# Kernel tuning notes

Hardware: AMD Instinct MI355X
Metric: run time of the kernel (lower is better)

The kernel has to match this reference:

```python
import jax, jax.numpy as jnp
import numpy as np


def setup_inputs() -> dict:
    key = jax.random.key(0)
    ks = jax.random.split(key, 5)
    B, Cin, Ch, H, W, K = 8, 64, 64, 128, 128, 3
    fan_in = (Cin + Ch) * K * K
    return {
        "x": jax.random.normal(ks[0], (B, Cin, H, W), jnp.float32),
        "prev_h": jax.random.normal(ks[1], (B, Ch, H, W), jnp.float32),
        "prev_c": jax.random.normal(ks[2], (B, Ch, H, W), jnp.float32),
        "W_gates": jax.random.normal(ks[3], (4 * Ch, Cin + Ch, K, K), jnp.float32) / np.sqrt(fan_in),
        "b_gates": jax.random.normal(ks[4], (4 * Ch,), jnp.float32) * 0.01,
    }


def reference(x, prev_h, prev_c, W_gates, b_gates):
    # ConvLSTM cell: conv over concat(input, prev_h) -> 4 gates -> gating.
    pad = W_gates.shape[-1] // 2
    stacked = jnp.concatenate([x, prev_h], axis=1)  # [B, Cin+Ch, H, W]
    gates = jax.lax.conv_general_dilated(
        stacked, W_gates,
        window_strides=(1, 1),
        padding=[(pad, pad), (pad, pad)],
        dimension_numbers=("NCHW", "OIHW", "NCHW"),
    ) + b_gates[None, :, None, None]  # [B, 4*Ch, H, W]
    in_gate, remember_gate, out_gate, cell_gate = jnp.split(gates, 4, axis=1)
    in_gate = jax.nn.sigmoid(in_gate)
    remember_gate = jax.nn.sigmoid(remember_gate)
    out_gate = jax.nn.sigmoid(out_gate)
    cell_gate = jnp.tanh(cell_gate)
    cell = in_gate * cell_gate + remember_gate * prev_c
    hidden = out_gate * jnp.tanh(cell)
    return (hidden, cell)
```

## Files before the change

### kernel.cpp

```cpp
#include <hip/hip_runtime.h>

typedef __attribute__((ext_vector_type(8))) short short8;
typedef __attribute__((ext_vector_type(4))) short short4v;
typedef __attribute__((ext_vector_type(4))) float float4v;

#define NPIX_HID 8388608
#define PST 132

__device__ __forceinline__ short f2bf(float f) {
    union { float f; unsigned u; } v; v.f = f;
    unsigned r = (v.u + 0x7FFFu + ((v.u >> 16) & 1u)) >> 16;
    return (short)r;
}

__device__ __forceinline__ float sigmoidf_(float v) { return 1.f / (1.f + __expf(-v)); }
__device__ __forceinline__ float tanhf_(float v)    { return 2.f / (1.f + __expf(-2.f * v)) - 1.f; }

__global__ void wprep(const float* __restrict__ W, short* __restrict__ A) {
    int tid = blockIdx.x * 256 + threadIdx.x;
    if (tid >= 9 * 16 * 256 * 8) return;
    int j   = tid & 7;
    int co  = (tid >> 3) & 255;
    int cig = (tid >> 11) & 15;
    int kk  = tid >> 15;
    int ci  = cig * 8 + j;
    A[tid] = f2bf(W[co * 1152 + ci * 9 + kk]);
}

#define ST_LOAD(P, II)                                                        \
  {                                                                           \
    const int i_ = (II);                                                      \
    P##_act = (i_ < 4224);                                                    \
    const int px_ = i_ % 66;                                                  \
    const int ro_ = i_ / 66;                                                  \
    P##_oct = ro_ & 15;                                                       \
    P##_row = ro_ >> 4;                                                       \
    const int ys_ = y0 + P##_row - 1;                                         \
    const int xs_ = x0 + px_ - 1;                                             \
    P##_px = px_;                                                             \
    P##_ok = P##_act & ((unsigned)ys_ < 128u) & ((unsigned)xs_ < 128u);       \
    const float* src_ = (P##_oct < 8) ? x : ph;                               \
    const float* sp_ = src_ + (P##_ok ?                                       \
        (((b * 64 + (P##_oct & 7) * 8) * 128 + ys_) * 128 + xs_) : 0);        \
    P##_v[0] = sp_[0];        P##_v[1] = sp_[16384];                          \
    P##_v[2] = sp_[2 * 16384]; P##_v[3] = sp_[3 * 16384];                     \
    P##_v[4] = sp_[4 * 16384]; P##_v[5] = sp_[5 * 16384];                     \
    P##_v[6] = sp_[6 * 16384]; P##_v[7] = sp_[7 * 16384];                     \
  }

#define ST_PROC(P)                                                            \
  if (P##_act) {                                                              \
    short4v lo_ = {0,0,0,0}, hi_ = {0,0,0,0};                                 \
    if (P##_ok) {                                                             \
      lo_[0] = f2bf(P##_v[0]); lo_[1] = f2bf(P##_v[1]);                       \
      lo_[2] = f2bf(P##_v[2]); lo_[3] = f2bf(P##_v[3]);                       \
      hi_[0] = f2bf(P##_v[4]); hi_[1] = f2bf(P##_v[5]);                       \
      hi_[2] = f2bf(P##_v[6]); hi_[3] = f2bf(P##_v[7]);                       \
    }                                                                         \
    short* dst_ = &Bs[(P##_row * 66 + P##_px) * PST + P##_oct * 8];           \
    *(short4v*)dst_       = lo_;                                              \
    *(short4v*)(dst_ + 4) = hi_;                                              \
  }

__global__ __launch_bounds__(256, 2) void convlstm_main(
    const float* __restrict__ x, const float* __restrict__ ph,
    const float* __restrict__ pc, const short* __restrict__ aprep,
    const float* __restrict__ bg, float* __restrict__ out)
{
    __shared__ short Bs[4 * 66 * PST];

    const int tid  = threadIdx.x;
    const int lane = tid & 63;
    const int wave = tid >> 6;
    const int l15  = lane & 15;
    const int quad = lane >> 4;

    const int t  = blockIdx.x;
    const int x0 = (t & 1) * 64;
    const int y0 = ((t >> 1) & 63) * 2;
    const int b  = t >> 7;

    {
        float stA_v[8]; int stA_px, stA_row, stA_oct; bool stA_ok, stA_act;
        float stB_v[8]; int stB_px, stB_row, stB_oct; bool stB_ok, stB_act;
        int ib = tid;
        ST_LOAD(stA, ib);
#pragma unroll 1
        for (int it = 0; it < 16; it += 2) {
            ST_LOAD(stB, ib + 256);
            ST_PROC(stA);
            ST_LOAD(stA, ib + 512);
            ST_PROC(stB);
            ib += 512;
        }
        ST_PROC(stA);
    }
    __syncthreads();

    float4v acc[4][8];
#pragma unroll
    for (int mt = 0; mt < 4; ++mt)
#pragma unroll
        for (int nt = 0; nt < 8; ++nt)
            acc[mt][nt] = (float4v){0.f, 0.f, 0.f, 0.f};

    const short* ap = aprep + quad * 2048 + (wave * 16 + l15) * 8;
    short8 abuf[2][4];
#pragma unroll
    for (int mt = 0; mt < 4; ++mt) abuf[0][mt] = *(const short8*)(ap + mt * 512);

    const short* bb = &Bs[l15 * PST + quad * 8];
    short8 bfr[2][8];
#pragma unroll
    for (int nt = 0; nt < 8; ++nt) {
        const short* bp = bb + (nt >> 2) * (66 * PST) + (nt & 3) * (16 * PST);
        short4v lo = *(const short4v*)bp;
        short4v hi = *(const short4v*)(bp + 4);
        bfr[0][nt] = __builtin_shufflevector(lo, hi, 0, 1, 2, 3, 4, 5, 6, 7);
    }

#pragma unroll 1
    for (int ky = 0; ky < 3; ++ky) {
#pragma unroll 1
        for (int kx = 0; kx < 3; ++kx) {
            const bool lastkx = (ky == 2) & (kx == 2);
            const short* bbn = bb + ((kx == 2) ? 64 * PST : PST);
#pragma unroll
            for (int kc = 0; kc < 4; ++kc) {
                const int cur = kc & 1, nxt = cur ^ 1;
                const bool last = lastkx & (kc == 3);

                const short* apn = last ? ap : (ap + 8192);
#pragma unroll
                for (int mt = 0; mt < 4; ++mt)
                    abuf[nxt][mt] = *(const short8*)(apn + mt * 512);
                ap = apn;

                const short* bq = (kc == 3) ? (lastkx ? bb : bbn) : bb;
                const int kcn = (kc + 1) & 3;
#pragma unroll
                for (int nt = 0; nt < 8; ++nt) {
                    const short* bp = bq + (nt >> 2) * (66 * PST) + (nt & 3) * (16 * PST) + kcn * 32;
                    short4v lo = *(const short4v*)bp;
                    short4v hi = *(const short4v*)(bp + 4);
                    bfr[nxt][nt] = __builtin_shufflevector(lo, hi, 0, 1, 2, 3, 4, 5, 6, 7);
                }

                __builtin_amdgcn_s_setprio(1);
#pragma unroll
                for (int mt = 0; mt < 4; ++mt)
#pragma unroll
                    for (int nt = 0; nt < 8; ++nt)
                        acc[mt][nt] = __builtin_amdgcn_mfma_f32_16x16x32_bf16(
                            abuf[cur][mt], bfr[cur][nt], acc[mt][nt], 0, 0, 0);
                __builtin_amdgcn_s_setprio(0);
            }
            bb = bbn;
        }
    }

    float pcv[8][4];
#pragma unroll
    for (int nt = 0; nt < 8; ++nt) {
        const int y  = y0 + (nt >> 2);
        const int px = x0 + ((nt & 3) << 4) + l15;
#pragma unroll
        for (int r = 0; r < 4; ++r) {
            const int c = wave * 16 + quad * 4 + r;
            pcv[nt][r] = pc[((b * 64 + c) * 128 + y) * 128 + px];
        }
    }
#pragma unroll
    for (int nt = 0; nt < 8; ++nt) {
        const int y  = y0 + (nt >> 2);
        const int px = x0 + ((nt & 3) << 4) + l15;
#pragma unroll
        for (int r = 0; r < 4; ++r) {
            const int c = wave * 16 + quad * 4 + r;
            const float gi = acc[0][nt][r] + bg[c];
            const float gf = acc[1][nt][r] + bg[64 + c];
            const float go = acc[2][nt][r] + bg[128 + c];
            const float gc = acc[3][nt][r] + bg[192 + c];
            const float ig = sigmoidf_(gi);
            const float fg = sigmoidf_(gf);
            const float og = sigmoidf_(go);
            const float cg = tanhf_(gc);
            const int idx = ((b * 64 + c) * 128 + y) * 128 + px;
            const float cell = ig * cg + fg * pcv[nt][r];
            const float hid  = og * tanhf_(cell);
            out[idx] = hid;
            out[NPIX_HID + idx] = cell;
        }
    }
}

extern "C" void kernel_launch(void* const* d_in, const int* in_sizes, int n_in,
                              void* d_out, int out_size, void* d_ws, size_t ws_size,
                              hipStream_t stream) {
    const float* x  = (const float*)d_in[0];
    const float* ph = (const float*)d_in[1];
    const float* pc = (const float*)d_in[2];
    const float* W  = (const float*)d_in[3];
    const float* bg = (const float*)d_in[4];
    float* out = (float*)d_out;
    short* aprep = (short*)d_ws;

    wprep<<<1152, 256, 0, stream>>>(W, aprep);
    convlstm_main<<<1024, 256, 0, stream>>>(x, ph, pc, aprep, bg, out);
}
```

Baseline: 209.3 us.

## Process four output rows per block with a rolling LDS row buffer

Each block now computes four output rows using a 4-slot circular shared-memory buffer of input rows. The next halo row is prefetched into registers during the current row's MFMA loop and written afterwards. This cuts redundant halo loads and fp32-to-bf16 conversion, and hoists the bias loads. In exchange the grid is halved, a barrier is added per row, and the per-wave N tile shrinks from 8 to 4, which lowers reuse of each A fragment.

```diff
diff --git a/kernel.cpp b/kernel.cpp
--- a/kernel.cpp
+++ b/kernel.cpp
@@ -6,6 +6,7 @@
 
 #define NPIX_HID 8388608
 #define PST 132
+#define ROWPITCH (66 * PST)
 
 __device__ __forceinline__ short f2bf(float f) {
     union { float f; unsigned u; } v; v.f = f;
@@ -27,10 +28,10 @@
     A[tid] = f2bf(W[co * 1152 + ci * 9 + kk]);
 }
 
-#define ST_LOAD(P, II)                                                        \
+#define PRO_LOAD(P, II)                                                       \
   {                                                                           \
     const int i_ = (II);                                                      \
-    P##_act = (i_ < 4224);                                                    \
+    P##_act = (i_ < 3168);                                                    \
     const int px_ = i_ % 66;                                                  \
     const int ro_ = i_ / 66;                                                  \
     P##_oct = ro_ & 15;                                                       \
@@ -42,24 +43,58 @@
     const float* src_ = (P##_oct < 8) ? x : ph;                               \
     const float* sp_ = src_ + (P##_ok ?                                       \
         (((b * 64 + (P##_oct & 7) * 8) * 128 + ys_) * 128 + xs_) : 0);        \
-    P##_v[0] = sp_[0];        P##_v[1] = sp_[16384];                          \
-    P##_v[2] = sp_[2 * 16384]; P##_v[3] = sp_[3 * 16384];                     \
-    P##_v[4] = sp_[4 * 16384]; P##_v[5] = sp_[5 * 16384];                     \
-    P##_v[6] = sp_[6 * 16384]; P##_v[7] = sp_[7 * 16384];                     \
-  }
-
-#define ST_PROC(P)                                                            \
+    P##_v[0]=sp_[0]; P##_v[1]=sp_[16384]; P##_v[2]=sp_[2*16384];              \
+    P##_v[3]=sp_[3*16384]; P##_v[4]=sp_[4*16384]; P##_v[5]=sp_[5*16384];      \
+    P##_v[6]=sp_[6*16384]; P##_v[7]=sp_[7*16384];                             \
+  }
+
+#define PRO_PROC(P)                                                           \
   if (P##_act) {                                                              \
-    short4v lo_ = {0,0,0,0}, hi_ = {0,0,0,0};                                 \
+    short4v lo_={0,0,0,0}, hi_={0,0,0,0};                                     \
     if (P##_ok) {                                                             \
-      lo_[0] = f2bf(P##_v[0]); lo_[1] = f2bf(P##_v[1]);                       \
-      lo_[2] = f2bf(P##_v[2]); lo_[3] = f2bf(P##_v[3]);                       \
-      hi_[0] = f2bf(P##_v[4]); hi_[1] = f2bf(P##_v[5]);                       \
-      hi_[2] = f2bf(P##_v[6]); hi_[3] = f2bf(P##_v[7]);                       \
+      lo_[0]=f2bf(P##_v[0]); lo_[1]=f2bf(P##_v[1]);                           \
+      lo_[2]=f2bf(P##_v[2]); lo_[3]=f2bf(P##_v[3]);                           \
+      hi_[0]=f2bf(P##_v[4]); hi_[1]=f2bf(P##_v[5]);                           \
+      hi_[2]=f2bf(P##_v[6]); hi_[3]=f2bf(P##_v[7]);                           \
     }                                                                         \
-    short* dst_ = &Bs[(P##_row * 66 + P##_px) * PST + P##_oct * 8];           \
-    *(short4v*)dst_       = lo_;                                              \
-    *(short4v*)(dst_ + 4) = hi_;                                              \
+    short* dst_ = &Bs[(((P##_row + 3) & 3) * 66 + P##_px) * PST + P##_oct * 8]; \
+    *(short4v*)dst_ = lo_; *(short4v*)(dst_+4) = hi_;                         \
+  }
+
+#define IST_LOAD(P, K)                                                        \
+  {                                                                           \
+    const int i_ = tid + (K) * 256;                                           \
+    const int px_ = i_ % 66;                                                  \
+    const int oct_ = (i_ / 66) & 15;                                          \
+    const int xs_ = x0 + px_ - 1;                                             \
+    const bool ok_ = (i_ < 1056) & ((unsigned)ysrc < 128u)                    \
+                     & ((unsigned)xs_ < 128u);                                \
+    const float* src_ = (oct_ < 8) ? x : ph;                                  \
+    const float* sp_ = src_ + (ok_ ?                                          \
+        (((b * 64 + (oct_ & 7) * 8) * 128 + ysrc) * 128 + xs_) : 0);          \
+    P##_v[0]=sp_[0]; P##_v[1]=sp_[16384]; P##_v[2]=sp_[2*16384];              \
+    P##_v[3]=sp_[3*16384]; P##_v[4]=sp_[4*16384]; P##_v[5]=sp_[5*16384];      \
+    P##_v[6]=sp_[6*16384]; P##_v[7]=sp_[7*16384];                             \
+  }
+
+#define IST_WRITE(P, K)                                                       \
+  {                                                                           \
+    const int i_ = tid + (K) * 256;                                           \
+    if (i_ < 1056) {                                                          \
+      const int px_ = i_ % 66;                                                \
+      const int oct_ = i_ / 66;                                               \
+      const int xs_ = x0 + px_ - 1;                                           \
+      const bool ok_ = ((unsigned)ysrc < 128u) & ((unsigned)xs_ < 128u);      \
+      short4v lo_={0,0,0,0}, hi_={0,0,0,0};                                   \
+      if (ok_) {                                                              \
+        lo_[0]=f2bf(P##_v[0]); lo_[1]=f2bf(P##_v[1]);                         \
+        lo_[2]=f2bf(P##_v[2]); lo_[3]=f2bf(P##_v[3]);                         \
+        hi_[0]=f2bf(P##_v[4]); hi_[1]=f2bf(P##_v[5]);                         \
+        hi_[2]=f2bf(P##_v[6]); hi_[3]=f2bf(P##_v[7]);                         \
+      }                                                                       \
+      short* dst_ = &Bs[(wslot * 66 + px_) * PST + oct_ * 8];                 \
+      *(short4v*)dst_ = lo_; *(short4v*)(dst_+4) = hi_;                       \
+    }                                                                         \
   }
 
 __global__ __launch_bounds__(256, 2) void convlstm_main(
@@ -67,7 +102,7 @@
     const float* __restrict__ pc, const short* __restrict__ aprep,
     const float* __restrict__ bg, float* __restrict__ out)
 {
-    __shared__ short Bs[4 * 66 * PST];
+    __shared__ short Bs[4 * ROWPITCH];
 
     const int tid  = threadIdx.x;
     const int lane = tid & 63;
@@ -77,119 +112,150 @@
 
     const int t  = blockIdx.x;
     const int x0 = (t & 1) * 64;
-    const int y0 = ((t >> 1) & 63) * 2;
-    const int b  = t >> 7;
+    const int y0 = ((t >> 1) & 31) * 4;
+    const int b  = t >> 6;
 
     {
-        float stA_v[8]; int stA_px, stA_row, stA_oct; bool stA_ok, stA_act;
-        float stB_v[8]; int stB_px, stB_row, stB_oct; bool stB_ok, stB_act;
+        float pA_v[8]; int pA_px, pA_row, pA_oct; bool pA_ok, pA_act;
+        float pB_v[8]; int pB_px, pB_row, pB_oct; bool pB_ok, pB_act;
         int ib = tid;
-        ST_LOAD(stA, ib);
-#pragma unroll 1
-        for (int it = 0; it < 16; it += 2) {
-            ST_LOAD(stB, ib + 256);
-            ST_PROC(stA);
-            ST_LOAD(stA, ib + 512);
-            ST_PROC(stB);
+        PRO_LOAD(pA, ib);
+#pragma unroll 1
+        for (int it = 0; it < 12; it += 2) {
+            PRO_LOAD(pB, ib + 256);
+            PRO_PROC(pA);
+            PRO_LOAD(pA, ib + 512);
+            PRO_PROC(pB);
             ib += 512;
         }
-        ST_PROC(stA);
+        PRO_PROC(pA);
     }
     __syncthreads();
 
-    float4v acc[4][8];
-#pragma unroll
-    for (int mt = 0; mt < 4; ++mt)
-#pragma unroll
-        for (int nt = 0; nt < 8; ++nt)
-            acc[mt][nt] = (float4v){0.f, 0.f, 0.f, 0.f};
-
-    const short* ap = aprep + quad * 2048 + (wave * 16 + l15) * 8;
+    const short* ap_base = aprep + quad * 2048 + (wave * 16 + l15) * 8;
+    const short* ap = ap_base;
     short8 abuf[2][4];
 #pragma unroll
-    for (int mt = 0; mt < 4; ++mt) abuf[0][mt] = *(const short8*)(ap + mt * 512);
-
-    const short* bb = &Bs[l15 * PST + quad * 8];
-    short8 bfr[2][8];
-#pragma unroll
-    for (int nt = 0; nt < 8; ++nt) {
-        const short* bp = bb + (nt >> 2) * (66 * PST) + (nt & 3) * (16 * PST);
+    for (int mt = 0; mt < 4; ++mt) abuf[0][mt] = *(const short8*)(ap_base + mt * 512);
+
+    const int lqoff = l15 * PST + quad * 8;
+    const short* bb = &Bs[3 * ROWPITCH + lqoff];
+    short8 bfr[2][4];
+#pragma unroll
+    for (int nt = 0; nt < 4; ++nt) {
+        const short* bp = bb + nt * (16 * PST);
         short4v lo = *(const short4v*)bp;
         short4v hi = *(const short4v*)(bp + 4);
         bfr[0][nt] = __builtin_shufflevector(lo, hi, 0, 1, 2, 3, 4, 5, 6, 7);
     }
 
-#pragma unroll 1
-    for (int ky = 0; ky < 3; ++ky) {
-#pragma unroll 1
-        for (int kx = 0; kx < 3; ++kx) {
-            const bool lastkx = (ky == 2) & (kx == 2);
-            const short* bbn = bb + ((kx == 2) ? 64 * PST : PST);
-#pragma unroll
-            for (int kc = 0; kc < 4; ++kc) {
-                const int cur = kc & 1, nxt = cur ^ 1;
-                const bool last = lastkx & (kc == 3);
-
-                const short* apn = last ? ap : (ap + 8192);
-#pragma unroll
-                for (int mt = 0; mt < 4; ++mt)
-                    abuf[nxt][mt] = *(const short8*)(apn + mt * 512);
-                ap = apn;
-
-                const short* bq = (kc == 3) ? (lastkx ? bb : bbn) : bb;
-                const int kcn = (kc + 1) & 3;
-#pragma unroll
-                for (int nt = 0; nt < 8; ++nt) {
-                    const short* bp = bq + (nt >> 2) * (66 * PST) + (nt & 3) * (16 * PST) + kcn * 32;
-                    short4v lo = *(const short4v*)bp;
-                    short4v hi = *(const short4v*)(bp + 4);
-                    bfr[nxt][nt] = __builtin_shufflevector(lo, hi, 0, 1, 2, 3, 4, 5, 6, 7);
+    float bgv[4][4];
+#pragma unroll
+    for (int g = 0; g < 4; ++g)
+#pragma unroll
+        for (int r = 0; r < 4; ++r)
+            bgv[g][r] = bg[g * 64 + wave * 16 + quad * 4 + r];
+
+#pragma unroll 1
+    for (int yy = 0; yy < 4; ++yy) {
+        const int ysrc  = y0 + yy + 2;
+        const int wslot = (yy + 2) & 3;
+        const short* bbnext = &Bs[(yy & 3) * ROWPITCH + lqoff];
+
+        float st0_v[8], st1_v[8], st2_v[8], st3_v[8], st4_v[8];
+        if (yy < 3) {
+            IST_LOAD(st0, 0) IST_LOAD(st1, 1) IST_LOAD(st2, 2)
+            IST_LOAD(st3, 3) IST_LOAD(st4, 4)
+        }
+        const int y = y0 + yy;
+        float pcv[4][4];
+#pragma unroll
+        for (int nt = 0; nt < 4; ++nt) {
+            const int px = x0 + (nt << 4) + l15;
+#pragma unroll
+            for (int r = 0; r < 4; ++r) {
+                const int c = wave * 16 + quad * 4 + r;
+                pcv[nt][r] = pc[((b * 64 + c) * 128 + y) * 128 + px];
+            }
+        }
+
+        float4v acc[4][4];
+#pragma unroll
+        for (int mt = 0; mt < 4; ++mt)
+#pragma unroll
+            for (int nt = 0; nt < 4; ++nt)
+                acc[mt][nt] = (float4v){0.f, 0.f, 0.f, 0.f};
+
+#pragma unroll 1
+        for (int ky = 0; ky < 3; ++ky) {
+            const int scur = (yy + ky + 3) & 3;
+            const int snxt = (yy + ky) & 3;
+            const int dj = (snxt - scur) * 66 - 2;
+#pragma unroll 1
+            for (int kx = 0; kx < 3; ++kx) {
+                const bool lastkx = (ky == 2) & (kx == 2);
+                const short* bbn = bb + ((kx == 2) ? dj * PST : PST);
+#pragma unroll
+                for (int kc = 0; kc < 4; ++kc) {
+                    const int cur = kc & 1, nxt = cur ^ 1;
+                    const bool last = lastkx & (kc == 3);
+
+                    const short* apn = last ? ap_base : (ap + 8192);
+#pragma unroll
+                    for (int mt = 0; mt < 4; ++mt)
+                        abuf[nxt][mt] = *(const short8*)(apn + mt * 512);
+                    ap = apn;
+
+                    const short* bq = (kc == 3) ? (lastkx ? bbnext : bbn) : bb;
+                    const int kcn = (kc + 1) & 3;
+#pragma unroll
+                    for (int nt = 0; nt < 4; ++nt) {
+                        const short* bp = bq + nt * (16 * PST) + kcn * 32;
+                        short4v lo = *(const short4v*)bp;
+                        short4v hi = *(const short4v*)(bp + 4);
+                        bfr[nxt][nt] = __builtin_shufflevector(lo, hi, 0, 1, 2, 3, 4, 5, 6, 7);
+                    }
+
+                    __builtin_amdgcn_s_setprio(1);
+#pragma unroll
+                    for (int mt = 0; mt < 4; ++mt)
+#pragma unroll
+                        for (int nt = 0; nt < 4; ++nt)
+                            acc[mt][nt] = __builtin_amdgcn_mfma_f32_16x16x32_bf16(
+                                abuf[cur][mt], bfr[cur][nt], acc[mt][nt], 0, 0, 0);
+                    __builtin_amdgcn_s_setprio(0);
                 }
-
-                __builtin_amdgcn_s_setprio(1);
-#pragma unroll
-                for (int mt = 0; mt < 4; ++mt)
-#pragma unroll
-                    for (int nt = 0; nt < 8; ++nt)
-                        acc[mt][nt] = __builtin_amdgcn_mfma_f32_16x16x32_bf16(
-                            abuf[cur][mt], bfr[cur][nt], acc[mt][nt], 0, 0, 0);
-                __builtin_amdgcn_s_setprio(0);
+                bb = bbn;
             }
-            bb = bbn;
-        }
-    }
-
-    float pcv[8][4];
-#pragma unroll
-    for (int nt = 0; nt < 8; ++nt) {
-        const int y  = y0 + (nt >> 2);
-        const int px = x0 + ((nt & 3) << 4) + l15;
-#pragma unroll
-        for (int r = 0; r < 4; ++r) {
-            const int c = wave * 16 + quad * 4 + r;
-            pcv[nt][r] = pc[((b * 64 + c) * 128 + y) * 128 + px];
-        }
-    }
-#pragma unroll
-    for (int nt = 0; nt < 8; ++nt) {
-        const int y  = y0 + (nt >> 2);
-        const int px = x0 + ((nt & 3) << 4) + l15;
-#pragma unroll
-        for (int r = 0; r < 4; ++r) {
-            const int c = wave * 16 + quad * 4 + r;
-            const float gi = acc[0][nt][r] + bg[c];
-            const float gf = acc[1][nt][r] + bg[64 + c];
-            const float go = acc[2][nt][r] + bg[128 + c];
-            const float gc = acc[3][nt][r] + bg[192 + c];
-            const float ig = sigmoidf_(gi);
-            const float fg = sigmoidf_(gf);
-            const float og = sigmoidf_(go);
-            const float cg = tanhf_(gc);
-            const int idx = ((b * 64 + c) * 128 + y) * 128 + px;
-            const float cell = ig * cg + fg * pcv[nt][r];
-            const float hid  = og * tanhf_(cell);
-            out[idx] = hid;
-            out[NPIX_HID + idx] = cell;
+        }
+        bb = bbnext;
+
+        if (yy < 3) {
+            IST_WRITE(st0, 0) IST_WRITE(st1, 1) IST_WRITE(st2, 2)
+            IST_WRITE(st3, 3) IST_WRITE(st4, 4)
+        }
+        __syncthreads();
+
+#pragma unroll
+        for (int nt = 0; nt < 4; ++nt) {
+            const int px = x0 + (nt << 4) + l15;
+#pragma unroll
+            for (int r = 0; r < 4; ++r) {
+                const int c = wave * 16 + quad * 4 + r;
+                const float gi = acc[0][nt][r] + bgv[0][r];
+                const float gf = acc[1][nt][r] + bgv[1][r];
+                const float go = acc[2][nt][r] + bgv[2][r];
+                const float gc = acc[3][nt][r] + bgv[3][r];
+                const float ig = sigmoidf_(gi);
+                const float fg = sigmoidf_(gf);
+                const float og = sigmoidf_(go);
+                const float cg = tanhf_(gc);
+                const int idx = ((b * 64 + c) * 128 + y) * 128 + px;
+                const float cell = ig * cg + fg * pcv[nt][r];
+                const float hid  = og * tanhf_(cell);
+                out[idx] = hid;
+                out[NPIX_HID + idx] = cell;
+            }
         }
     }
 }
@@ -206,5 +272,5 @@
     short* aprep = (short*)d_ws;
 
     wprep<<<1152, 256, 0, stream>>>(W, aprep);
-    convlstm_main<<<1024, 256, 0, stream>>>(x, ph, pc, aprep, bg, out);
-}
+    convlstm_main<<<512, 256, 0, stream>>>(x, ph, pc, aprep, bg, out);
+}
```

New measurement: 264.7 us. 1.26x slower.
